# Optimization experiments

Hardware: AMD Instinct MI355X
Metric: run time of the kernel (lower is better)

Reference implementation:

```python
import jax, jax.numpy as jnp
import numpy as np

B, T, H, L, FUT = 64, 256, 512, 4, 64


def setup_inputs() -> dict:
    key = jax.random.key(0)
    ks = jax.random.split(key, 8)
    s = 1.0 / np.sqrt(H)  # PyTorch LSTMCell/Linear default uniform init bound
    u = lambda k, shape: jax.random.uniform(k, shape, jnp.float32, -s, s)
    return {
        "iput": jax.random.normal(ks[0], (B, T), jnp.float32),
        "W_ih0": u(ks[1], (4 * H, 1)),        # layer 0 input->gates
        "W_ih": u(ks[2], (L - 1, 4 * H, H)),  # layers 1..L-1 input->gates
        "W_hh": u(ks[3], (L, 4 * H, H)),      # hidden->gates, all layers
        "b_ih": u(ks[4], (L, 4 * H)),
        "b_hh": u(ks[5], (L, 4 * H)),
        "W_lin": u(ks[6], (1, H)),            # readout Linear(H, 1)
        "b_lin": u(ks[7], (1,)),
        "future": FUT,
    }


def _cell(x, h, c, Wi, Wh, bi, bh):
    # PyTorch LSTMCell: gates ordered i, f, g, o
    g = x @ Wi.T + h @ Wh.T + bi + bh  # [B, 4H]
    i, f, gg, o = jnp.split(g, 4, axis=-1)
    c2 = jax.nn.sigmoid(f) * c + jax.nn.sigmoid(i) * jnp.tanh(gg)
    h2 = jax.nn.sigmoid(o) * jnp.tanh(c2)
    return h2, c2


def reference(iput, W_ih0, W_ih, W_hh, b_ih, b_hh, W_lin, b_lin, future):
    Lc = W_hh.shape[0]
    Bsz = iput.shape[0]
    Hd = W_hh.shape[-1]

    def layers(x, hs, cs):  # x: [B,1]; hs,cs: [L,B,H]
        for j in range(Lc):
            Wi = W_ih0 if j == 0 else W_ih[j - 1]
            inp = x if j == 0 else hs[j - 1]
            h2, c2 = _cell(inp, hs[j], cs[j], Wi, W_hh[j], b_ih[j], b_hh[j])
            hs = hs.at[j].set(h2)
            cs = cs.at[j].set(c2)
        return hs, cs

    hs0 = jnp.zeros((Lc, Bsz, Hd), iput.dtype)
    cs0 = jnp.zeros_like(hs0)

    def step_in(carry, x_t):  # x_t: [B]
        hs, cs = carry
        hs, cs = layers(x_t[:, None], hs, cs)
        out = hs[-1] @ W_lin.T + b_lin  # [B,1]
        return (hs, cs), out[:, 0]

    (hs, cs), outs = jax.lax.scan(step_in, (hs0, cs0), iput.T)  # outs: [T,B]

    def step_fut(carry, _):
        hs, cs, out = carry
        hs, cs = layers(out, hs, cs)
        out2 = hs[-1] @ W_lin.T + b_lin
        return (hs, cs, out2), out2[:, 0]

    last_out = outs[-1][:, None]  # feed last prediction back
    _, fouts = jax.lax.scan(step_fut, (hs, cs, last_out), None, length=future)

    return jnp.concatenate([outs, fouts], axis=0).T  # [B, T+future]
```

## Files before the change

### kernel.cpp

```cpp
#include <hip/hip_runtime.h>

#define Bsz 64
#define Tn 256
#define Hn 512
#define Ln 4
#define Gn 2048
#define TTn 320
#define NBLK 256
#define NTHR 512
#define HB (Hn * Bsz)
#define LHB (Ln * HB)
#define NPH_W (Tn + Ln - 1)

typedef float f32x4 __attribute__((ext_vector_type(4)));

#define OFF_WHH  0
#define OFF_WIH  (OFF_WHH + Ln * 8 * Hn)
#define OFF_PART (OFF_WIH + (Ln - 1) * 8 * Hn)
#define OFF_GSUM (OFF_PART + 8 * 8 * Bsz)
#define OFF_BS   (OFF_GSUM + Ln * 8 * Bsz)
#define OFF_W0   (OFF_BS + Ln * 8)
#define OFF_WLIN (OFF_W0 + 8)
#define OFF_RP   (OFF_WLIN + Hn)
#define OFF_XS   (OFF_RP + 8 * Bsz)
#define OFF_C    (OFF_XS + Bsz)
#define SMEM_FLOATS (OFF_C + Ln * 2 * Bsz)
#define SMEM_BYTES (SMEM_FLOATS * 4)

#define WS_BCOUNT   0
#define WS_ARRIVE   16
#define WS_INVD     (16 + 16 * 32)
#define WS_MASTER   (16 + 32 * 32)
#define WS_FLAG     (WS_MASTER + 32)
#define WS_BOOT     (WS_FLAG + 32)
#define WS_BOOTFLAG (WS_BOOT + 32)
#define WS_U32S     (WS_BOOTFLAG + 32)

__device__ float g_h[2 * LHB];
__device__ float g_hist[Tn * HB];
__device__ float g_p[Bsz * NBLK];
__device__ float g_xsg[Bsz];

__device__ __forceinline__ float sigm(float x) { return 1.0f / (1.0f + expf(-x)); }

__device__ __forceinline__ void fma4v(f32x4& a, const f32x4 h, const float w) {
    a.x = fmaf(h.x, w, a.x); a.y = fmaf(h.y, w, a.y);
    a.z = fmaf(h.z, w, a.z); a.w = fmaf(h.w, w, a.w);
}

#define GSTF(ptr, val) \
    asm volatile("global_store_dword %0, %1, off sc0 sc1" \
                 :: "v"(ptr), "v"(val) : "memory")
#define VMWAIT() asm volatile("s_waitcnt vmcnt(0)" ::: "memory")
#define L1INV() asm volatile("buffer_inv" ::: "memory")

__device__ __forceinline__ uint32_t rmw_add(uint32_t* p, uint32_t v) {
    return __hip_atomic_fetch_add(p, v, __ATOMIC_RELAXED, __HIP_MEMORY_SCOPE_AGENT);
}
__device__ __forceinline__ uint32_t ald(const uint32_t* p) {
    return __hip_atomic_load(p, __ATOMIC_RELAXED, __HIP_MEMORY_SCOPE_AGENT);
}
__device__ __forceinline__ uint32_t xcc_id() {
    uint32_t x;
    asm("s_getreg_b32 %0, hwreg(HW_REG_XCC_ID)" : "=s"(x));
    return x & 15u;
}

__device__ __forceinline__ void boot_bar(uint32_t* wsb, int tid) {
    VMWAIT();
    __syncthreads();
    if (tid == 0) {
        __builtin_amdgcn_fence(__ATOMIC_RELEASE, "agent");
        uint32_t old = rmw_add(wsb + WS_BOOT, 1u);
        if (old == NBLK - 1u) rmw_add(wsb + WS_BOOTFLAG, 1u);
        while (ald(wsb + WS_BOOTFLAG) < 1u) __builtin_amdgcn_s_sleep(2);
        __builtin_amdgcn_fence(__ATOMIC_ACQUIRE, "agent");
    }
    __syncthreads();
    asm volatile("" ::: "memory");
}

__device__ __forceinline__ void gbar(uint32_t* wsb, int tid, uint32_t x,
                                     uint32_t cnt_x, uint32_t& e) {
    ++e;
    VMWAIT();
    __syncthreads();
    if (tid == 0) {
        uint32_t old = rmw_add(wsb + WS_ARRIVE + x * 32, 1u);
        if (old == e * cnt_x - 1u) {
            __builtin_amdgcn_fence(__ATOMIC_ACQUIRE, "agent");
            VMWAIT();
            uint32_t m = rmw_add(wsb + WS_MASTER, cnt_x);
            if (m + cnt_x == e * (uint32_t)NBLK)
                rmw_add(wsb + WS_FLAG, 1u);
            while (ald(wsb + WS_FLAG) < e) __builtin_amdgcn_s_sleep(1);
            rmw_add(wsb + WS_INVD + x * 32, 1u);
        } else {
            while (ald(wsb + WS_INVD + x * 32) < e) {}
            L1INV();
            VMWAIT();
        }
    }
    __syncthreads();
    asm volatile("" ::: "memory");
}

__device__ __forceinline__ void gemm16(const float* __restrict__ w,
                                       const float* __restrict__ hbase,
                                       int k0, int b4, f32x4* acc) {
#pragma unroll
    for (int c = 0; c < 4; ++c) {
        const int k = k0 + c * 4;
        const float* hp = hbase + (size_t)k * Bsz + b4;
        const f32x4 h0 = *(const f32x4*)(hp);
        const f32x4 h1 = *(const f32x4*)(hp + Bsz);
        const f32x4 h2 = *(const f32x4*)(hp + 2 * Bsz);
        const f32x4 h3 = *(const f32x4*)(hp + 3 * Bsz);
#pragma unroll
        for (int r = 0; r < 8; ++r) {
            const f32x4 wv = *(const f32x4*)(w + r * Hn + k);
            fma4v(acc[r], h0, wv.x); fma4v(acc[r], h1, wv.y);
            fma4v(acc[r], h2, wv.z); fma4v(acc[r], h3, wv.w);
        }
    }
}

__global__ __launch_bounds__(NTHR, 1)
void lstm_seq(const float* __restrict__ iput,
              const float* __restrict__ Wih0,
              const float* __restrict__ Wih,
              const float* __restrict__ Whh,
              const float* __restrict__ bih,
              const float* __restrict__ bhh,
              const float* __restrict__ Wlin,
              const float* __restrict__ blin,
              float* __restrict__ out,
              uint32_t* __restrict__ wsb)
{
    extern __shared__ float sm[];
    const int bi  = blockIdx.x;
    const int tid = threadIdx.x;
    uint32_t e = 0;

    const uint32_t x = xcc_id();
    uint32_t cnt_x = 0;
    if (tid == 0) rmw_add(wsb + WS_BCOUNT + x, 1u);

    for (int i = tid; i < Ln * 8 * Hn; i += NTHR) {
        const int lyr = i >> 12, rem = i & 4095, r = rem >> 9, k = rem & 511;
        sm[OFF_WHH + i] = Whh[((size_t)(lyr * Gn + (r & 3) * Hn + bi * 2 + (r >> 2))) * Hn + k];
    }
    for (int i = tid; i < (Ln - 1) * 8 * Hn; i += NTHR) {
        const int lyr = i >> 12, rem = i & 4095, r = rem >> 9, k = rem & 511;
        sm[OFF_WIH + i] = Wih[((size_t)(lyr * Gn + (r & 3) * Hn + bi * 2 + (r >> 2))) * Hn + k];
    }
    if (tid < Ln * 8) {
        const int lyr = tid >> 3, r = tid & 7;
        const int gg = lyr * Gn + (r & 3) * Hn + bi * 2 + (r >> 2);
        sm[OFF_BS + tid] = bih[gg] + bhh[gg];
    }
    if (tid < 8) sm[OFF_W0 + tid] = Wih0[(tid & 3) * Hn + bi * 2 + (tid >> 2)];
    for (int i = tid; i < Hn; i += NTHR) sm[OFF_WLIN + i] = Wlin[i];
    for (int i = tid; i < Ln * 2 * Bsz; i += NTHR) sm[OFF_C + i] = 0.0f;

    for (int i = bi * NTHR + tid; i < 2 * LHB; i += NBLK * NTHR)
        GSTF(&g_h[i], 0.0f);

    const float blin0 = blin[0];
    boot_bar(wsb, tid);
    if (tid == 0) cnt_x = ald(wsb + WS_BCOUNT + x);

    {
        const int l   = tid >> 7;
        const int sub = tid & 127;
        const int bgw = sub & 15, b4w = bgw * 4;
        const int kgw = sub >> 4;
        const int k0w = kgw * 64;
        const int w2  = (tid >> 6) & 1;

        for (int s = 0; s < NPH_W; ++s) {
            const int pp = s & 1;
            float* cur        = g_h + pp * LHB;
            const float* prev = g_h + (pp ^ 1) * LHB;
            const int t = s - l;
            const bool act = ((unsigned)t < (unsigned)Tn);

            f32x4 acc[8];
#pragma unroll
            for (int r = 0; r < 8; ++r) acc[r] = (f32x4){0.f, 0.f, 0.f, 0.f};

            if (act) {
                {
                    const float* wh  = sm + OFF_WHH + l * 8 * Hn;
                    const float* hp0 = prev + (size_t)l * HB;
#pragma unroll 4
                    for (int c = 0; c < 16; ++c) {
                        const int k = k0w + (((c + (kgw & 3) * 4) & 15) << 2);
                        const float* hp = hp0 + (size_t)k * Bsz + b4w;
                        const f32x4 h0 = *(const f32x4*)(hp);
                        const f32x4 h1 = *(const f32x4*)(hp + Bsz);
                        const f32x4 h2 = *(const f32x4*)(hp + 2 * Bsz);
                        const f32x4 h3 = *(const f32x4*)(hp + 3 * Bsz);
#pragma unroll
                        for (int r = 0; r < 8; ++r) {
                            const f32x4 wv = *(const f32x4*)(wh + r * Hn + k);
                            fma4v(acc[r], h0, wv.x); fma4v(acc[r], h1, wv.y);
                            fma4v(acc[r], h2, wv.z); fma4v(acc[r], h3, wv.w);
                        }
                    }
                }
                if (l > 0) {
                    const float* wh  = sm + OFF_WIH + (l - 1) * 8 * Hn;
                    const float* hp0 = prev + (size_t)(l - 1) * HB;
#pragma unroll 4
                    for (int c = 0; c < 16; ++c) {
                        const int k = k0w + (((c + (kgw & 3) * 4) & 15) << 2);
                        const float* hp = hp0 + (size_t)k * Bsz + b4w;
                        const f32x4 h0 = *(const f32x4*)(hp);
                        const f32x4 h1 = *(const f32x4*)(hp + Bsz);
                        const f32x4 h2 = *(const f32x4*)(hp + 2 * Bsz);
                        const f32x4 h3 = *(const f32x4*)(hp + 3 * Bsz);
#pragma unroll
                        for (int r = 0; r < 8; ++r) {
                            const f32x4 wv = *(const f32x4*)(wh + r * Hn + k);
                            fma4v(acc[r], h0, wv.x); fma4v(acc[r], h1, wv.y);
                            fma4v(acc[r], h2, wv.z); fma4v(acc[r], h3, wv.w);
                        }
                    }
                }
            }

#pragma unroll
            for (int r = 0; r < 8; ++r) {
                f32x4 a = acc[r];
                a.x += __shfl_xor(a.x, 16); a.y += __shfl_xor(a.y, 16);
                a.z += __shfl_xor(a.z, 16); a.w += __shfl_xor(a.w, 16);
                a.x += __shfl_xor(a.x, 32); a.y += __shfl_xor(a.y, 32);
                a.z += __shfl_xor(a.z, 32); a.w += __shfl_xor(a.w, 32);
                acc[r] = a;
            }
            if ((tid & 48) == 0) {
#pragma unroll
                for (int r = 0; r < 8; ++r)
                    *(f32x4*)&sm[OFF_PART + ((l * 2 + w2) * 8 + r) * Bsz + b4w] = acc[r];
            }
            __syncthreads();

#pragma unroll
            for (int it = 0; it < 4; ++it) {
                const int idx = it * NTHR + tid;
                const int la = idx >> 9, r = (idx >> 6) & 7, b = idx & 63;
                float v = sm[OFF_BS + la * 8 + r]
                        + sm[OFF_PART + ((la * 2 + 0) * 8 + r) * Bsz + b]
                        + sm[OFF_PART + ((la * 2 + 1) * 8 + r) * Bsz + b];
                if (la == 0 && s < Tn)
                    v = fmaf(iput[b * Tn + s], sm[OFF_W0 + r], v);
                sm[OFF_GSUM + idx] = v;
            }
            __syncthreads();

            {
                const int lb = tid >> 7, jl = (tid >> 6) & 1, b = tid & 63;
                const int tb = s - lb;
                if ((unsigned)tb < (unsigned)Tn) {
                    const int jg = bi * 2 + jl;
                    const float* gs = sm + OFF_GSUM + lb * 512 + (jl << 2) * 64;
                    const float i_ = sigm(gs[0 * 64 + b]);
                    const float f_ = sigm(gs[1 * 64 + b]);
                    const float g_ = tanhf(gs[2 * 64 + b]);
                    const float o_ = sigm(gs[3 * 64 + b]);
                    float* cp = sm + OFF_C + (lb * 2 + jl) * Bsz + b;
                    const float c2 = fmaf(f_, *cp, i_ * g_);
                    *cp = c2;
                    const float h2 = o_ * tanhf(c2);
                    GSTF(&cur[((size_t)lb * Hn + jg) * Bsz + b], h2);
                    if (lb == 3)
                        GSTF(&g_hist[((size_t)tb * Hn + jg) * Bsz + b], h2);
                }
            }
            gbar(wsb, tid, x, cnt_x, e);
        }
    }

    {
        const int b = tid & 63, jq = tid >> 6;
        const float* hp = g_hist + ((size_t)bi * Hn + jq * 64) * Bsz + b;
        const float* wp = sm + OFF_WLIN + jq * 64;
        float r = 0.0f;
#pragma unroll 8
        for (int j = 0; j < 64; ++j) r = fmaf(hp[j * Bsz], wp[j], r);
        sm[OFF_RP + jq * Bsz + b] = r;
        if (tid < 256) {
            const int li = (tid >> 7) * 2 + 1;
            const int jl = (tid >> 6) & 1, bb = tid & 63;
            const size_t o = ((size_t)li * Hn + bi * 2 + jl) * Bsz + bb;
            const float v = g_h[o];
            GSTF(&g_h[LHB + o], v);
        }
        __syncthreads();
        if (tid < Bsz) {
            float xx = blin0;
#pragma unroll
            for (int q = 0; q < 8; ++q) xx += sm[OFF_RP + q * Bsz + tid];
            out[tid * TTn + bi] = xx;
            if (bi == 255) GSTF(&g_xsg[tid], xx);
        }
        gbar(wsb, tid, x, cnt_x, e);
    }

    {
        const int bg  = tid & 15, b4 = bg * 4;
        const int kg  = tid >> 4;
        const int k0  = kg * 16;
        const int wv_ = tid >> 6;

        for (int t = Tn; t < TTn; ++t) {
            const int ci = t & 1;
            float* hcur        = g_h + ci * LHB;
            const float* hprev = g_h + (ci ^ 1) * LHB;

            for (int lyr = 0; lyr < Ln; ++lyr) {
                if (lyr == 0 && tid < Bsz) {
                    float xx;
                    if (t == Tn) {
                        xx = g_xsg[tid];
                    } else {
                        const f32x4* pp2 = (const f32x4*)(g_p + tid * NBLK);
                        f32x4 s4 = {0.f, 0.f, 0.f, 0.f};
#pragma unroll 16
                        for (int q = 0; q < NBLK / 4; ++q) s4 += pp2[q];
                        xx = s4.x + s4.y + s4.z + s4.w + blin0;
                        if (bi == ((t - 1) & 255))
                            out[tid * TTn + (t - 1)] = xx;
                    }
                    sm[OFF_XS + tid] = xx;
                }

                f32x4 acc[8];
#pragma unroll
                for (int r = 0; r < 8; ++r) acc[r] = (f32x4){0.f, 0.f, 0.f, 0.f};

                if (lyr > 0)
                    gemm16(sm + OFF_WIH + (lyr - 1) * 8 * Hn,
                           hcur + (size_t)(lyr - 1) * HB, k0, b4, acc);
                gemm16(sm + OFF_WHH + lyr * 8 * Hn,
                       hprev + (size_t)lyr * HB, k0, b4, acc);

#pragma unroll
                for (int r = 0; r < 8; ++r) {
                    f32x4 a = acc[r];
                    a.x += __shfl_xor(a.x, 16); a.y += __shfl_xor(a.y, 16);
                    a.z += __shfl_xor(a.z, 16); a.w += __shfl_xor(a.w, 16);
                    a.x += __shfl_xor(a.x, 32); a.y += __shfl_xor(a.y, 32);
                    a.z += __shfl_xor(a.z, 32); a.w += __shfl_xor(a.w, 32);
                    acc[r] = a;
                }
                if ((tid & 48) == 0) {
#pragma unroll
                    for (int r = 0; r < 8; ++r)
                        *(f32x4*)&sm[OFF_PART + (wv_ * 8 + r) * Bsz + b4] = acc[r];
                }
                __syncthreads();

                {
                    const int r = tid >> 6, b = tid & 63;
                    float v = sm[OFF_BS + lyr * 8 + r];
#pragma unroll
                    for (int q = 0; q < 8; ++q)
                        v += sm[OFF_PART + (q * 8 + r) * Bsz + b];
                    if (lyr == 0)
                        v = fmaf(sm[OFF_XS + b], sm[OFF_W0 + r], v);
                    sm[OFF_GSUM + tid] = v;
                }
                __syncthreads();

                float h2 = 0.0f;
                if (tid < 128) {
                    const int jl = tid >> 6, b = tid & 63;
                    const int jg = bi * 2 + jl;
                    const float* gs = sm + OFF_GSUM + jl * 4 * Bsz;
                    const float i_ = sigm(gs[0 * Bsz + b]);
                    const float f_ = sigm(gs[1 * Bsz + b]);
                    const float g_ = tanhf(gs[2 * Bsz + b]);
                    const float o_ = sigm(gs[3 * Bsz + b]);
                    float* cp = sm + OFF_C + (lyr * 2 + jl) * Bsz + b;
                    const float c2 = fmaf(f_, *cp, i_ * g_);
                    *cp = c2;
                    h2 = o_ * tanhf(c2);
                    GSTF(&hcur[((size_t)lyr * Hn + jg) * Bsz + b], h2);
                    if (lyr == 3 && jl == 1)
                        sm[OFF_RP + b] = h2 * sm[OFF_WLIN + jg];
                }
                __syncthreads();
                if (lyr == 3 && tid < Bsz) {
                    const float pv = fmaf(h2, sm[OFF_WLIN + bi * 2], sm[OFF_RP + tid]);
                    GSTF(&g_p[tid * NBLK + bi], pv);
                }

                gbar(wsb, tid, x, cnt_x, e);
            }
        }
    }

    if (bi == 0 && tid < Bsz) {
        const f32x4* pp2 = (const f32x4*)(g_p + tid * NBLK);
        f32x4 s4 = {0.f, 0.f, 0.f, 0.f};
#pragma unroll 16
        for (int q = 0; q < NBLK / 4; ++q) s4 += pp2[q];
        out[tid * TTn + (TTn - 1)] = s4.x + s4.y + s4.z + s4.w + blin0;
    }
}

extern "C" void kernel_launch(void* const* d_in, const int* in_sizes, int n_in,
                              void* d_out, int out_size, void* d_ws, size_t ws_size,
                              hipStream_t stream) {
    const float* iput = (const float*)d_in[0];
    const float* Wih0 = (const float*)d_in[1];
    const float* Wih  = (const float*)d_in[2];
    const float* Whh  = (const float*)d_in[3];
    const float* bih  = (const float*)d_in[4];
    const float* bhh  = (const float*)d_in[5];
    const float* Wlin = (const float*)d_in[6];
    const float* blin = (const float*)d_in[7];
    float* out = (float*)d_out;
    uint32_t* wsb = (uint32_t*)d_ws;

    (void)hipFuncSetAttribute((const void*)lstm_seq,
                              hipFuncAttributeMaxDynamicSharedMemorySize, SMEM_BYTES);

    (void)hipMemsetAsync(d_ws, 0, WS_U32S * sizeof(uint32_t), stream);

    void* args[] = {&iput, &Wih0, &Wih, &Whh, &bih, &bhh, &Wlin, &blin, &out, &wsb};
    hipLaunchCooperativeKernel((const void*)lstm_seq, dim3(NBLK), dim3(NTHR), args,
                               SMEM_BYTES, stream);
}
```

Before: 9.109 ms.

## Flatten grid barrier to single counter and fuse gate reduction into cell update

The two-level grid barrier, which used a master flag plus per-group invalidate counters, becomes a single global counter that every block spins on directly. This removes one release hop per barrier. The gate-sum staging buffer in shared memory and its __syncthreads are removed: each cell thread now reduces its own four gate partials in registers. The extra block sync in the future phase now runs only on the last layer. In exchange, all 256 blocks poll one shared atomic, which adds contention, and fewer threads do the reduction work.

Result: no change. 9.115 ms (+0.1%).

```diff
diff --git a/kernel.cpp b/kernel.cpp
--- a/kernel.cpp
+++ b/kernel.cpp
@@ -17,8 +17,7 @@
 #define OFF_WHH  0
 #define OFF_WIH  (OFF_WHH + Ln * 8 * Hn)
 #define OFF_PART (OFF_WIH + (Ln - 1) * 8 * Hn)
-#define OFF_GSUM (OFF_PART + 8 * 8 * Bsz)
-#define OFF_BS   (OFF_GSUM + Ln * 8 * Bsz)
+#define OFF_BS   (OFF_PART + 8 * 8 * Bsz)
 #define OFF_W0   (OFF_BS + Ln * 8)
 #define OFF_WLIN (OFF_W0 + 8)
 #define OFF_RP   (OFF_WLIN + Hn)
@@ -29,10 +28,8 @@
 
 #define WS_BCOUNT   0
 #define WS_ARRIVE   16
-#define WS_INVD     (16 + 16 * 32)
-#define WS_MASTER   (16 + 32 * 32)
-#define WS_FLAG     (WS_MASTER + 32)
-#define WS_BOOT     (WS_FLAG + 32)
+#define WS_MASTER   (16 + 16 * 32)
+#define WS_BOOT     (WS_MASTER + 32)
 #define WS_BOOTFLAG (WS_BOOT + 32)
 #define WS_U32S     (WS_BOOTFLAG + 32)
 
@@ -86,17 +83,15 @@
     VMWAIT();
     __syncthreads();
     if (tid == 0) {
+        const uint32_t tgt = e * (uint32_t)NBLK;
         uint32_t old = rmw_add(wsb + WS_ARRIVE + x * 32, 1u);
         if (old == e * cnt_x - 1u) {
             __builtin_amdgcn_fence(__ATOMIC_ACQUIRE, "agent");
             VMWAIT();
-            uint32_t m = rmw_add(wsb + WS_MASTER, cnt_x);
-            if (m + cnt_x == e * (uint32_t)NBLK)
-                rmw_add(wsb + WS_FLAG, 1u);
-            while (ald(wsb + WS_FLAG) < e) __builtin_amdgcn_s_sleep(1);
-            rmw_add(wsb + WS_INVD + x * 32, 1u);
+            rmw_add(wsb + WS_MASTER, cnt_x);
+            while (ald(wsb + WS_MASTER) < tgt) {}
         } else {
-            while (ald(wsb + WS_INVD + x * 32) < e) {}
+            while (ald(wsb + WS_MASTER) < tgt) {}
             L1INV();
             VMWAIT();
         }
@@ -246,29 +241,29 @@
             }
             __syncthreads();
 
-#pragma unroll
-            for (int it = 0; it < 4; ++it) {
-                const int idx = it * NTHR + tid;
-                const int la = idx >> 9, r = (idx >> 6) & 7, b = idx & 63;
-                float v = sm[OFF_BS + la * 8 + r]
-                        + sm[OFF_PART + ((la * 2 + 0) * 8 + r) * Bsz + b]
-                        + sm[OFF_PART + ((la * 2 + 1) * 8 + r) * Bsz + b];
-                if (la == 0 && s < Tn)
-                    v = fmaf(iput[b * Tn + s], sm[OFF_W0 + r], v);
-                sm[OFF_GSUM + idx] = v;
-            }
-            __syncthreads();
-
             {
                 const int lb = tid >> 7, jl = (tid >> 6) & 1, b = tid & 63;
                 const int tb = s - lb;
                 if ((unsigned)tb < (unsigned)Tn) {
                     const int jg = bi * 2 + jl;
-                    const float* gs = sm + OFF_GSUM + lb * 512 + (jl << 2) * 64;
-                    const float i_ = sigm(gs[0 * 64 + b]);
-                    const float f_ = sigm(gs[1 * 64 + b]);
-                    const float g_ = tanhf(gs[2 * 64 + b]);
-                    const float o_ = sigm(gs[3 * 64 + b]);
+                    float gv[4];
+#pragma unroll
+                    for (int q = 0; q < 4; ++q) {
+                        const int r = (jl << 2) | q;
+                        gv[q] = sm[OFF_BS + lb * 8 + r]
+                              + sm[OFF_PART + ((lb * 2 + 0) * 8 + r) * Bsz + b]
+                              + sm[OFF_PART + ((lb * 2 + 1) * 8 + r) * Bsz + b];
+                    }
+                    if (lb == 0) {
+                        const float xv = iput[b * Tn + s];
+#pragma unroll
+                        for (int q = 0; q < 4; ++q)
+                            gv[q] = fmaf(xv, sm[OFF_W0 + ((jl << 2) | q)], gv[q]);
+                    }
+                    const float i_ = sigm(gv[0]);
+                    const float f_ = sigm(gv[1]);
+                    const float g_ = tanhf(gv[2]);
+                    const float o_ = sigm(gv[3]);
                     float* cp = sm + OFF_C + (lb * 2 + jl) * Bsz + b;
                     const float c2 = fmaf(f_, *cp, i_ * g_);
                     *cp = c2;
@@ -362,27 +357,26 @@
                 }
                 __syncthreads();
 
-                {
-                    const int r = tid >> 6, b = tid & 63;
-                    float v = sm[OFF_BS + lyr * 8 + r];
-#pragma unroll
-                    for (int q = 0; q < 8; ++q)
-                        v += sm[OFF_PART + (q * 8 + r) * Bsz + b];
-                    if (lyr == 0)
-                        v = fmaf(sm[OFF_XS + b], sm[OFF_W0 + r], v);
-                    sm[OFF_GSUM + tid] = v;
-                }
-                __syncthreads();
-
                 float h2 = 0.0f;
                 if (tid < 128) {
                     const int jl = tid >> 6, b = tid & 63;
                     const int jg = bi * 2 + jl;
-                    const float* gs = sm + OFF_GSUM + jl * 4 * Bsz;
-                    const float i_ = sigm(gs[0 * Bsz + b]);
-                    const float f_ = sigm(gs[1 * Bsz + b]);
-                    const float g_ = tanhf(gs[2 * Bsz + b]);
-                    const float o_ = sigm(gs[3 * Bsz + b]);
+                    float gv[4];
+#pragma unroll
+                    for (int q = 0; q < 4; ++q) {
+                        const int r = (jl << 2) | q;
+                        float v = sm[OFF_BS + lyr * 8 + r];
+#pragma unroll
+                        for (int p = 0; p < 8; ++p)
+                            v += sm[OFF_PART + (p * 8 + r) * Bsz + b];
+                        if (lyr == 0)
+                            v = fmaf(sm[OFF_XS + b], sm[OFF_W0 + r], v);
+                        gv[q] = v;
+                    }
+                    const float i_ = sigm(gv[0]);
+                    const float f_ = sigm(gv[1]);
+                    const float g_ = tanhf(gv[2]);
+                    const float o_ = sigm(gv[3]);
                     float* cp = sm + OFF_C + (lyr * 2 + jl) * Bsz + b;
                     const float c2 = fmaf(f_, *cp, i_ * g_);
                     *cp = c2;
@@ -391,10 +385,12 @@
                     if (lyr == 3 && jl == 1)
                         sm[OFF_RP + b] = h2 * sm[OFF_WLIN + jg];
                 }
-                __syncthreads();
-                if (lyr == 3 && tid < Bsz) {
-                    const float pv = fmaf(h2, sm[OFF_WLIN + bi * 2], sm[OFF_RP + tid]);
-                    GSTF(&g_p[tid * NBLK + bi], pv);
+                if (lyr == 3) {
+                    __syncthreads();
+                    if (tid < Bsz) {
+                        const float pv = fmaf(h2, sm[OFF_WLIN + bi * 2], sm[OFF_RP + tid]);
+                        GSTF(&g_p[tid * NBLK + bi], pv);
+                    }
                 }
 
                 gbar(wsb, tid, x, cnt_x, e);
```
